# Performance work log

Hardware: AMD Instinct MI355X
Metric: run time of the kernel (lower is better)

Reference implementation:

```python
import jax, jax.numpy as jnp
import numpy as np

EPS = 1e-12  # matches torch euclidean_dist clamp(min=1e-12)


def _euclidean_dist(a, b):
    # pairwise sqrt distances: [N, M]
    d2 = (jnp.sum(a * a, axis=1)[:, None]
          + jnp.sum(b * b, axis=1)[None, :]
          - 2.0 * (a @ b.T))
    return jnp.sqrt(jnp.clip(d2, EPS))


def setup_inputs() -> dict:
    key = jax.random.key(0)
    k1, k2, k3 = jax.random.split(key, 3)
    B, I, E, C = 131072, 512, 128, 64
    x = jax.random.normal(k1, (B, I), dtype=jnp.float32)
    y = jax.random.randint(k2, (B,), 0, C)  # class labels
    W = jax.random.normal(k3, (E, I), dtype=jnp.float32) * 0.02
    b = jnp.zeros((E,), dtype=jnp.float32)
    centroid = jnp.zeros((C, E), dtype=jnp.float32)
    return {"x": x, "y": y, "W": W, "b": b, "centroid": centroid}


def reference(x, y, W, b, centroid):
    # linear projection: [B, E]
    out = x @ W.T + b
    C = centroid.shape[0]
    # fused per-class masked mean (segment mean). flag[i]==0 always in the
    # original module, so the executed update is centroid[i] += mean_i.
    sums = jax.ops.segment_sum(out, y, num_segments=C)            # [C, E]
    counts = jax.ops.segment_sum(jnp.ones(y.shape, out.dtype), y,
                                 num_segments=C)                   # [C]
    means = sums / counts[:, None]
    new_centroid = centroid + means
    # only the final loop iteration's proto_dist / dist survive
    proto_dist = jnp.exp(-0.5 * _euclidean_dist(new_centroid, new_centroid))
    dist = _euclidean_dist(out, new_centroid)                      # [B, C]
    return jax.nn.sigmoid(jnp.exp(-0.5 * dist)), proto_dist
```

## Files before the change

kernel.cpp:

```cpp
#include <hip/hip_runtime.h>
#include <math.h>


typedef __bf16 bf16;
typedef bf16  bf16x4 __attribute__((ext_vector_type(4)));
typedef bf16  bf16x8 __attribute__((ext_vector_type(8)));
typedef float f32x4  __attribute__((ext_vector_type(4)));

#define B_ROWS 131072
#define K_DIM  512
#define E_DIM  128
#define C_CLS  64

#define BM 128
#define BN 128
#define BK 64

#define SEG_BLOCKS 256
#define ROWS_PER_SEG (B_ROWS / SEG_BLOCKS)

__global__ __launch_bounds__(256, 2)
void gemm_kernel(const float* __restrict__ x, const float* __restrict__ W,
                 const float* __restrict__ bias, float* __restrict__ out)
{
    __shared__ bf16 As[BM * BK];
    __shared__ bf16 Bs[BN * BK];

    const int t    = threadIdx.x;
    const int lane = t & 63;
    const int w    = t >> 6;
    const int wr   = w >> 1;
    const int wc   = w & 1;
    const int fr   = lane & 15;
    const int fq   = lane >> 4;
    const long blockRow = (long)blockIdx.x * BM;

    const int srow = t >> 4;
    const int scol = (t & 15) * 4;

    f32x4 acc[4][4] = {};

    const float* xg = x + blockRow * K_DIM;

    for (int kt = 0; kt < K_DIM; kt += BK) {
        __syncthreads();
        #pragma unroll
        for (int r = 0; r < 8; ++r) {
            int row = r * 16 + srow;
            f32x4 va = *(const f32x4*)(xg + (long)row * K_DIM + kt + scol);
            f32x4 vb = *(const f32x4*)(W  + (long)row * K_DIM + kt + scol);
            bf16x4 pa = { (bf16)va.x, (bf16)va.y, (bf16)va.z, (bf16)va.w };
            bf16x4 pb = { (bf16)vb.x, (bf16)vb.y, (bf16)vb.z, (bf16)vb.w };
            int byte = row * (BK * 2) + ((scol * 2) ^ ((row & 7) << 4));
            *(bf16x4*)((char*)As + byte) = pa;
            *(bf16x4*)((char*)Bs + byte) = pb;
        }
        __syncthreads();
        #pragma unroll
        for (int kk = 0; kk < 2; ++kk) {
            bf16x8 af[4], bg[4];
            #pragma unroll
            for (int m = 0; m < 4; ++m) {
                int row  = wr * 64 + m * 16 + fr;
                int byte = row * (BK * 2) + (((kk * 32 + fq * 8) * 2) ^ ((row & 7) << 4));
                af[m] = *(const bf16x8*)((const char*)As + byte);
            }
            #pragma unroll
            for (int n = 0; n < 4; ++n) {
                int row  = wc * 64 + n * 16 + fr;
                int byte = row * (BK * 2) + (((kk * 32 + fq * 8) * 2) ^ ((row & 7) << 4));
                bg[n] = *(const bf16x8*)((const char*)Bs + byte);
            }
            #pragma unroll
            for (int m = 0; m < 4; ++m)
                #pragma unroll
                for (int n = 0; n < 4; ++n)
                    acc[m][n] = __builtin_amdgcn_mfma_f32_16x16x32_bf16(
                        af[m], bg[n], acc[m][n], 0, 0, 0);
        }
    }

    #pragma unroll
    for (int n = 0; n < 4; ++n) {
        int gcol = wc * 64 + n * 16 + fr;
        float bv = bias[gcol];
        #pragma unroll
        for (int m = 0; m < 4; ++m) {
            #pragma unroll
            for (int j = 0; j < 4; ++j) {
                long grow = blockRow + wr * 64 + m * 16 + fq * 4 + j;
                out[grow * E_DIM + gcol] = acc[m][n][j] + bv;
            }
        }
    }
}

__global__ __launch_bounds__(256)
void segsum_kernel(const float* __restrict__ out, const int* __restrict__ y,
                   float* __restrict__ pw, float* __restrict__ pc)
{
    __shared__ float lsum[C_CLS * E_DIM];
    __shared__ float lcnt[C_CLS];
    const int t = threadIdx.x;
    for (int i = t; i < C_CLS * E_DIM; i += 256) lsum[i] = 0.f;
    if (t < C_CLS) lcnt[t] = 0.f;
    __syncthreads();
    const long base = (long)blockIdx.x * ROWS_PER_SEG;
    for (int r = t; r < ROWS_PER_SEG; r += 256)
        atomicAdd(&lcnt[y[base + r]], 1.0f);
    const int rsub = t >> 5;
    const int c4   = (t & 31) * 4;
    for (int i = 0; i < ROWS_PER_SEG; i += 8) {
        long row = base + i + rsub;
        int  cls = y[row];
        f32x4 v = *(const f32x4*)(out + row * E_DIM + c4);
        atomicAdd(&lsum[cls * E_DIM + c4 + 0], v.x);
        atomicAdd(&lsum[cls * E_DIM + c4 + 1], v.y);
        atomicAdd(&lsum[cls * E_DIM + c4 + 2], v.z);
        atomicAdd(&lsum[cls * E_DIM + c4 + 3], v.w);
    }
    __syncthreads();
    for (int i = t; i < C_CLS * E_DIM; i += 256)
        pw[(long)blockIdx.x * (C_CLS * E_DIM) + i] = lsum[i];
    if (t < C_CLS) pc[blockIdx.x * C_CLS + t] = lcnt[t];
}

__global__ __launch_bounds__(256)
void reduce_kernel(const float* __restrict__ pw, float* __restrict__ sums)
{
    int idx = blockIdx.x * 256 + threadIdx.x;
    float s = 0.f;
    for (int j = 0; j < SEG_BLOCKS; ++j) s += pw[(long)j * (C_CLS * E_DIM) + idx];
    sums[idx] = s;
}

__global__ __launch_bounds__(256)
void centroid_kernel(const float* __restrict__ sums, const float* __restrict__ pc,
                     const float* __restrict__ centroid0,
                     float* __restrict__ cent, float* __restrict__ cnorm)
{
    __shared__ float cnt[C_CLS];
    __shared__ float sc[C_CLS * E_DIM];
    const int t = threadIdx.x;
    if (t < C_CLS) {
        float s = 0.f;
        for (int j = 0; j < SEG_BLOCKS; ++j) s += pc[j * C_CLS + t];
        cnt[t] = s;
    }
    __syncthreads();
    for (int i = t; i < C_CLS * E_DIM; i += 256) {
        float v = centroid0[i] + sums[i] / cnt[i >> 7];
        sc[i]   = v;
        cent[i] = v;
    }
    __syncthreads();
    if (t < C_CLS) {
        float s = 0.f;
        for (int e = 0; e < E_DIM; ++e) { float v = sc[t * E_DIM + e]; s += v * v; }
        cnorm[t] = s;
    }
}

__global__ __launch_bounds__(256)
void proto_kernel(const float* __restrict__ cent, const float* __restrict__ cnorm,
                  float* __restrict__ proto)
{
    __shared__ float sc[C_CLS * E_DIM];
    const int t = threadIdx.x;
    for (int i = t; i < C_CLS * E_DIM; i += 256) sc[i] = cent[i];
    __syncthreads();
    int p = blockIdx.x * 256 + t;
    int i = p >> 6, j = p & 63;
    float d = 0.f;
    for (int e = 0; e < E_DIM; ++e) d += sc[i * E_DIM + e] * sc[j * E_DIM + e];
    float d2 = cnorm[i] + cnorm[j] - 2.f * d;
    proto[p] = __expf(-0.5f * sqrtf(fmaxf(d2, 1e-12f)));
}

__global__ __launch_bounds__(256, 4)
void dist_kernel(const float* __restrict__ out, const float* __restrict__ cent,
                 const float* __restrict__ cnorm, float* __restrict__ out0)
{
    __shared__ bf16  Cs[C_CLS * E_DIM];
    __shared__ float snorm[C_CLS];
    __shared__ float rnorm[128];
    const int t = threadIdx.x;
    {
        int srow = t >> 5;
        int scol = (t & 31) * 4;
        #pragma unroll
        for (int r = 0; r < 8; ++r) {
            int row = r * 8 + srow;
            f32x4 v = *(const f32x4*)(cent + row * E_DIM + scol);
            bf16x4 pv = { (bf16)v.x, (bf16)v.y, (bf16)v.z, (bf16)v.w };
            int byte = row * (E_DIM * 2) + ((scol * 2) ^ ((row & 7) << 4));
            *(bf16x4*)((char*)Cs + byte) = pv;
        }
        if (t < C_CLS) snorm[t] = cnorm[t];
    }
    const int lane = t & 63;
    const int w    = t >> 6;
    const int fr   = lane & 15;
    const int fq   = lane >> 4;
    const long blkrow = (long)blockIdx.x * 128;
    f32x4 acc[2][4] = {};
    float sq0 = 0.f, sq1 = 0.f;
    __syncthreads();
    #pragma unroll
    for (int kt = 0; kt < 4; ++kt) {
        bf16x8 af[2];
        #pragma unroll
        for (int m = 0; m < 2; ++m) {
            long row = blkrow + w * 32 + m * 16 + fr;
            const f32x4* p = (const f32x4*)(out + row * E_DIM + kt * 32 + fq * 8);
            f32x4 v0 = p[0];
            f32x4 v1 = p[1];
            float s = v0.x*v0.x + v0.y*v0.y + v0.z*v0.z + v0.w*v0.w
                    + v1.x*v1.x + v1.y*v1.y + v1.z*v1.z + v1.w*v1.w;
            if (m == 0) sq0 += s; else sq1 += s;
            bf16x8 a;
            a[0]=(bf16)v0.x; a[1]=(bf16)v0.y; a[2]=(bf16)v0.z; a[3]=(bf16)v0.w;
            a[4]=(bf16)v1.x; a[5]=(bf16)v1.y; a[6]=(bf16)v1.z; a[7]=(bf16)v1.w;
            af[m] = a;
        }
        #pragma unroll
        for (int n = 0; n < 4; ++n) {
            int row  = n * 16 + fr;
            int byte = row * (E_DIM * 2) + (((kt * 32 + fq * 8) * 2) ^ ((row & 7) << 4));
            bf16x8 bq = *(const bf16x8*)((const char*)Cs + byte);
            acc[0][n] = __builtin_amdgcn_mfma_f32_16x16x32_bf16(af[0], bq, acc[0][n], 0, 0, 0);
            acc[1][n] = __builtin_amdgcn_mfma_f32_16x16x32_bf16(af[1], bq, acc[1][n], 0, 0, 0);
        }
    }
    sq0 += __shfl_xor(sq0, 16); sq0 += __shfl_xor(sq0, 32);
    sq1 += __shfl_xor(sq1, 16); sq1 += __shfl_xor(sq1, 32);
    if (fq == 0) {
        rnorm[w * 32 + fr]      = sq0;
        rnorm[w * 32 + 16 + fr] = sq1;
    }
    __syncthreads();
    #pragma unroll
    for (int m = 0; m < 2; ++m) {
        #pragma unroll
        for (int n = 0; n < 4; ++n) {
            int gcol = n * 16 + fr;
            float cn = snorm[gcol];
            #pragma unroll
            for (int j = 0; j < 4; ++j) {
                int lrow = w * 32 + m * 16 + fq * 4 + j;
                float d2 = rnorm[lrow] + cn - 2.f * acc[m][n][j];
                float dist = sqrtf(fmaxf(d2, 1e-12f));
                float ez = __expf(-0.5f * dist);
                out0[(blkrow + lrow) * C_CLS + gcol] = 1.f / (1.f + __expf(-ez));
            }
        }
    }
}

extern "C" void kernel_launch(void* const* d_in, const int* in_sizes, int n_in,
                              void* d_out, int out_size, void* d_ws, size_t ws_size,
                              hipStream_t stream)
{
    const float* x         = (const float*)d_in[0];
    const int*   y         = (const int*)d_in[1];
    const float* W         = (const float*)d_in[2];
    const float* bias      = (const float*)d_in[3];
    const float* centroid0 = (const float*)d_in[4];

    float* outb  = (float*)d_ws;
    float* pw    = outb + (long)B_ROWS * E_DIM;
    float* pc    = pw + (long)SEG_BLOCKS * C_CLS * E_DIM;
    float* sums  = pc + SEG_BLOCKS * C_CLS;
    float* cent  = sums + C_CLS * E_DIM;
    float* cnorm = cent + C_CLS * E_DIM;

    float* out0  = (float*)d_out;
    float* proto = out0 + (long)B_ROWS * C_CLS;

    gemm_kernel    <<<B_ROWS / BM, 256, 0, stream>>>(x, W, bias, outb);
    segsum_kernel  <<<SEG_BLOCKS, 256, 0, stream>>>(outb, y, pw, pc);
    reduce_kernel  <<<(C_CLS * E_DIM) / 256, 256, 0, stream>>>(pw, sums);
    centroid_kernel<<<1, 256, 0, stream>>>(sums, pc, centroid0, cent, cnorm);
    proto_kernel   <<<(C_CLS * C_CLS) / 256, 256, 0, stream>>>(cent, cnorm, proto);
    dist_kernel    <<<B_ROWS / 128, 256, 0, stream>>>(outb, cent, cnorm, out0);
}
```

Baseline: 230.5 us.

## Store projection as bf16 with fused row norms; merge proto into dist kernel

The GEMM epilogue now writes the projected activations as bf16 instead of fp32 and computes per-row squared norms in the epilogue via shuffles and shared atomics. This halves the intermediate write and its two re-reads in segsum and dist. Segsum reads bf16x8 vectors and folds the class counting into the main loop. The proto computation is folded into extra blocks of the dist kernel, which removes one launch. In exchange, segment sums are now taken over bf16-rounded values, which reduces precision.

```diff
diff --git a/kernel.cpp b/kernel.cpp
--- a/kernel.cpp
+++ b/kernel.cpp
@@ -13,18 +13,22 @@
 #define C_CLS  64
 
 #define BM 128
-#define BN 128
 #define BK 64
 
 #define SEG_BLOCKS 256
 #define ROWS_PER_SEG (B_ROWS / SEG_BLOCKS)
 
+#define DIST_BLOCKS (B_ROWS / 128)
+#define PROTO_BLOCKS 16
+
 __global__ __launch_bounds__(256, 2)
 void gemm_kernel(const float* __restrict__ x, const float* __restrict__ W,
-                 const float* __restrict__ bias, float* __restrict__ out)
+                 const float* __restrict__ bias, bf16* __restrict__ outb,
+                 float* __restrict__ rnorm)
 {
     __shared__ bf16 As[BM * BK];
-    __shared__ bf16 Bs[BN * BK];
+    __shared__ bf16 Bs[BM * BK];
+    __shared__ float lr[BM];
 
     const int t    = threadIdx.x;
     const int lane = t & 63;
@@ -39,6 +43,7 @@
     const int scol = (t & 15) * 4;
 
     f32x4 acc[4][4] = {};
+    if (t < BM) lr[t] = 0.f;
 
     const float* xg = x + blockRow * K_DIM;
 
@@ -80,23 +85,33 @@
         }
     }
 
-    #pragma unroll
-    for (int n = 0; n < 4; ++n) {
-        int gcol = wc * 64 + n * 16 + fr;
-        float bv = bias[gcol];
-        #pragma unroll
-        for (int m = 0; m < 4; ++m) {
-            #pragma unroll
-            for (int j = 0; j < 4; ++j) {
-                long grow = blockRow + wr * 64 + m * 16 + fq * 4 + j;
-                out[grow * E_DIM + gcol] = acc[m][n][j] + bv;
-            }
-        }
-    }
+    float bvv[4];
+    #pragma unroll
+    for (int n = 0; n < 4; ++n) bvv[n] = bias[wc * 64 + n * 16 + fr];
+
+    #pragma unroll
+    for (int m = 0; m < 4; ++m) {
+        #pragma unroll
+        for (int j = 0; j < 4; ++j) {
+            long grow = blockRow + wr * 64 + m * 16 + fq * 4 + j;
+            float s = 0.f;
+            #pragma unroll
+            for (int n = 0; n < 4; ++n) {
+                float v = acc[m][n][j] + bvv[n];
+                outb[grow * E_DIM + wc * 64 + n * 16 + fr] = (bf16)v;
+                s += v * v;
+            }
+            s += __shfl_xor(s, 1); s += __shfl_xor(s, 2);
+            s += __shfl_xor(s, 4); s += __shfl_xor(s, 8);
+            if (fr == 0) atomicAdd(&lr[wr * 64 + m * 16 + fq * 4 + j], s);
+        }
+    }
+    __syncthreads();
+    if (t < BM) rnorm[blockRow + t] = lr[t];
 }
 
 __global__ __launch_bounds__(256)
-void segsum_kernel(const float* __restrict__ out, const int* __restrict__ y,
+void segsum_kernel(const bf16* __restrict__ outb, const int* __restrict__ y,
                    float* __restrict__ pw, float* __restrict__ pc)
 {
     __shared__ float lsum[C_CLS * E_DIM];
@@ -106,18 +121,16 @@
     if (t < C_CLS) lcnt[t] = 0.f;
     __syncthreads();
     const long base = (long)blockIdx.x * ROWS_PER_SEG;
-    for (int r = t; r < ROWS_PER_SEG; r += 256)
-        atomicAdd(&lcnt[y[base + r]], 1.0f);
-    const int rsub = t >> 5;
-    const int c4   = (t & 31) * 4;
-    for (int i = 0; i < ROWS_PER_SEG; i += 8) {
+    const int rsub = t >> 4;
+    const int c8   = (t & 15) * 8;
+    for (int i = 0; i < ROWS_PER_SEG; i += 16) {
         long row = base + i + rsub;
         int  cls = y[row];
-        f32x4 v = *(const f32x4*)(out + row * E_DIM + c4);
-        atomicAdd(&lsum[cls * E_DIM + c4 + 0], v.x);
-        atomicAdd(&lsum[cls * E_DIM + c4 + 1], v.y);
-        atomicAdd(&lsum[cls * E_DIM + c4 + 2], v.z);
-        atomicAdd(&lsum[cls * E_DIM + c4 + 3], v.w);
+        bf16x8 v = *(const bf16x8*)(outb + row * E_DIM + c8);
+        if ((t & 15) == 0) atomicAdd(&lcnt[cls], 1.0f);
+        #pragma unroll
+        for (int k = 0; k < 8; ++k)
+            atomicAdd(&lsum[cls * E_DIM + c8 + k], (float)v[k]);
     }
     __syncthreads();
     for (int i = t; i < C_CLS * E_DIM; i += 256)
@@ -161,42 +174,49 @@
     }
 }
 
-__global__ __launch_bounds__(256)
-void proto_kernel(const float* __restrict__ cent, const float* __restrict__ cnorm,
-                  float* __restrict__ proto)
-{
-    __shared__ float sc[C_CLS * E_DIM];
+__global__ __launch_bounds__(256, 4)
+void dist_kernel(const bf16* __restrict__ outb, const float* __restrict__ cent,
+                 const float* __restrict__ cnorm, const float* __restrict__ rnorm,
+                 float* __restrict__ out0, float* __restrict__ proto)
+{
+    __shared__ float smemf[C_CLS * 129 + C_CLS + 128];
     const int t = threadIdx.x;
-    for (int i = t; i < C_CLS * E_DIM; i += 256) sc[i] = cent[i];
-    __syncthreads();
-    int p = blockIdx.x * 256 + t;
-    int i = p >> 6, j = p & 63;
-    float d = 0.f;
-    for (int e = 0; e < E_DIM; ++e) d += sc[i * E_DIM + e] * sc[j * E_DIM + e];
-    float d2 = cnorm[i] + cnorm[j] - 2.f * d;
-    proto[p] = __expf(-0.5f * sqrtf(fmaxf(d2, 1e-12f)));
-}
-
-__global__ __launch_bounds__(256, 4)
-void dist_kernel(const float* __restrict__ out, const float* __restrict__ cent,
-                 const float* __restrict__ cnorm, float* __restrict__ out0)
-{
-    __shared__ bf16  Cs[C_CLS * E_DIM];
-    __shared__ float snorm[C_CLS];
-    __shared__ float rnorm[128];
-    const int t = threadIdx.x;
+
+    if (blockIdx.x >= DIST_BLOCKS) {
+        float* scf   = smemf;
+        float* pnorm = smemf + C_CLS * 129;
+        for (int idx = t; idx < C_CLS * E_DIM; idx += 256)
+            scf[(idx >> 7) * 129 + (idx & 127)] = cent[idx];
+        if (t < C_CLS) pnorm[t] = cnorm[t];
+        __syncthreads();
+        int p = (blockIdx.x - DIST_BLOCKS) * 256 + t;
+        int i = p >> 6, j = p & 63;
+        float d = 0.f;
+        #pragma unroll 4
+        for (int e = 0; e < E_DIM; ++e)
+            d += scf[i * 129 + e] * scf[j * 129 + e];
+        float d2 = pnorm[i] + pnorm[j] - 2.f * d;
+        proto[p] = __expf(-0.5f * sqrtf(fmaxf(d2, 1e-12f)));
+        return;
+    }
+
+    bf16*  Cs    = (bf16*)smemf;
+    float* snorm = smemf + C_CLS * 129;
+    float* srnorm = snorm + C_CLS;
     {
-        int srow = t >> 5;
-        int scol = (t & 31) * 4;
+        int srw = t >> 5;
+        int scl = (t & 31) * 4;
         #pragma unroll
         for (int r = 0; r < 8; ++r) {
-            int row = r * 8 + srow;
-            f32x4 v = *(const f32x4*)(cent + row * E_DIM + scol);
+            int row = r * 8 + srw;
+            f32x4 v = *(const f32x4*)(cent + row * E_DIM + scl);
             bf16x4 pv = { (bf16)v.x, (bf16)v.y, (bf16)v.z, (bf16)v.w };
-            int byte = row * (E_DIM * 2) + ((scol * 2) ^ ((row & 7) << 4));
+            int byte = row * (E_DIM * 2) + ((scl * 2) ^ ((row & 7) << 4));
             *(bf16x4*)((char*)Cs + byte) = pv;
         }
         if (t < C_CLS) snorm[t] = cnorm[t];
+        if (t < 32) ((f32x4*)srnorm)[t] =
+            ((const f32x4*)(rnorm + (long)blockIdx.x * 128))[t];
     }
     const int lane = t & 63;
     const int w    = t >> 6;
@@ -204,7 +224,6 @@
     const int fq   = lane >> 4;
     const long blkrow = (long)blockIdx.x * 128;
     f32x4 acc[2][4] = {};
-    float sq0 = 0.f, sq1 = 0.f;
     __syncthreads();
     #pragma unroll
     for (int kt = 0; kt < 4; ++kt) {
@@ -212,16 +231,7 @@
         #pragma unroll
         for (int m = 0; m < 2; ++m) {
             long row = blkrow + w * 32 + m * 16 + fr;
-            const f32x4* p = (const f32x4*)(out + row * E_DIM + kt * 32 + fq * 8);
-            f32x4 v0 = p[0];
-            f32x4 v1 = p[1];
-            float s = v0.x*v0.x + v0.y*v0.y + v0.z*v0.z + v0.w*v0.w
-                    + v1.x*v1.x + v1.y*v1.y + v1.z*v1.z + v1.w*v1.w;
-            if (m == 0) sq0 += s; else sq1 += s;
-            bf16x8 a;
-            a[0]=(bf16)v0.x; a[1]=(bf16)v0.y; a[2]=(bf16)v0.z; a[3]=(bf16)v0.w;
-            a[4]=(bf16)v1.x; a[5]=(bf16)v1.y; a[6]=(bf16)v1.z; a[7]=(bf16)v1.w;
-            af[m] = a;
+            af[m] = *(const bf16x8*)(outb + row * E_DIM + kt * 32 + fq * 8);
         }
         #pragma unroll
         for (int n = 0; n < 4; ++n) {
@@ -232,13 +242,6 @@
             acc[1][n] = __builtin_amdgcn_mfma_f32_16x16x32_bf16(af[1], bq, acc[1][n], 0, 0, 0);
         }
     }
-    sq0 += __shfl_xor(sq0, 16); sq0 += __shfl_xor(sq0, 32);
-    sq1 += __shfl_xor(sq1, 16); sq1 += __shfl_xor(sq1, 32);
-    if (fq == 0) {
-        rnorm[w * 32 + fr]      = sq0;
-        rnorm[w * 32 + 16 + fr] = sq1;
-    }
-    __syncthreads();
     #pragma unroll
     for (int m = 0; m < 2; ++m) {
         #pragma unroll
@@ -248,7 +251,7 @@
             #pragma unroll
             for (int j = 0; j < 4; ++j) {
                 int lrow = w * 32 + m * 16 + fq * 4 + j;
-                float d2 = rnorm[lrow] + cn - 2.f * acc[m][n][j];
+                float d2 = srnorm[lrow] + cn - 2.f * acc[m][n][j];
                 float dist = sqrtf(fmaxf(d2, 1e-12f));
                 float ez = __expf(-0.5f * dist);
                 out0[(blkrow + lrow) * C_CLS + gcol] = 1.f / (1.f + __expf(-ez));
@@ -267,8 +270,9 @@
     const float* bias      = (const float*)d_in[3];
     const float* centroid0 = (const float*)d_in[4];
 
-    float* outb  = (float*)d_ws;
-    float* pw    = outb + (long)B_ROWS * E_DIM;
+    bf16*  outb  = (bf16*)d_ws;
+    float* rnorm = (float*)((char*)d_ws + (size_t)B_ROWS * E_DIM * 2);
+    float* pw    = rnorm + B_ROWS;
     float* pc    = pw + (long)SEG_BLOCKS * C_CLS * E_DIM;
     float* sums  = pc + SEG_BLOCKS * C_CLS;
     float* cent  = sums + C_CLS * E_DIM;
@@ -277,10 +281,10 @@
     float* out0  = (float*)d_out;
     float* proto = out0 + (long)B_ROWS * C_CLS;
 
-    gemm_kernel    <<<B_ROWS / BM, 256, 0, stream>>>(x, W, bias, outb);
+    gemm_kernel    <<<B_ROWS / BM, 256, 0, stream>>>(x, W, bias, outb, rnorm);
     segsum_kernel  <<<SEG_BLOCKS, 256, 0, stream>>>(outb, y, pw, pc);
     reduce_kernel  <<<(C_CLS * E_DIM) / 256, 256, 0, stream>>>(pw, sums);
     centroid_kernel<<<1, 256, 0, stream>>>(sums, pc, centroid0, cent, cnorm);
-    proto_kernel   <<<(C_CLS * C_CLS) / 256, 256, 0, stream>>>(cent, cnorm, proto);
-    dist_kernel    <<<B_ROWS / 128, 256, 0, stream>>>(outb, cent, cnorm, out0);
-}
+    dist_kernel    <<<DIST_BLOCKS + PROTO_BLOCKS, 256, 0, stream>>>(
+        outb, cent, cnorm, rnorm, out0, proto);
+}
```

Measured after the change: 192.9 us. -16.3%, faster.
